# Kernel tuning notes

Measured on AMD Instinct MI355X. Metric: run time of the kernel, lower is better.

## Reference

```python
import math
import jax, jax.numpy as jnp
import numpy as np

B, S, D, H = 2, 2048, 2048, 16
HD = D // H  # head_dim = 128, rotary_dim = HD (full rotation)
ROPE_BASE = 10000.0


def setup_inputs() -> dict:
    key = jax.random.key(0)
    k0, k1, k2 = jax.random.split(key, 3)
    return {
        "x": jax.random.normal(k0, (B, S, D), dtype=jnp.float32),
        "Wqkv": jax.random.normal(k1, (D, 3 * D), dtype=jnp.float32) * 0.02,
        "bqkv": jnp.zeros((3 * D,), dtype=jnp.float32),
        "Wout": jax.random.normal(k2, (D, D), dtype=jnp.float32) * 0.02,
        "bout": jnp.zeros((D,), dtype=jnp.float32),
    }


def _rope_cos_sin(seqlen, dim):
    # flash-attn RotaryEmbedding: inv_freq over even indices, outer with positions
    inv_freq = 1.0 / (ROPE_BASE ** (jnp.arange(0, dim, 2, dtype=jnp.float32) / dim))
    t = jnp.arange(seqlen, dtype=jnp.float32)
    freqs = jnp.outer(t, inv_freq)  # (S, dim/2)
    return jnp.cos(freqs), jnp.sin(freqs)


def reference(x, Wqkv, bqkv, Wout, bout):
    b, s, d = x.shape
    hd = d // H
    # fused QKV projection -> (B, S, 3, H, HD)
    qkv = (x @ Wqkv + bqkv).reshape(b, s, 3, H, hd)
    q, k, v = qkv[:, :, 0], qkv[:, :, 1], qkv[:, :, 2]  # (B,S,H,HD)

    cos, sin = _rope_cos_sin(s, hd)
    c = cos[:, None, :]  # (S,1,HD/2) broadcast over heads
    si = sin[:, None, :]

    def rot(t):
        # split-half rotary (as in apply_rotary_emb_qkv), computed in fp32
        t1, t2 = jnp.split(t.astype(jnp.float32), 2, axis=-1)
        return jnp.concatenate([t1 * c - t2 * si, t1 * si + t2 * c], axis=-1).astype(x.dtype)

    q = rot(q)
    k = rot(k)

    scale = 1.0 / math.sqrt(hd)
    scores = jnp.einsum("bthd,bshd->bhts", q, k * scale)  # (B,H,S,S)
    causal_mask = jnp.triu(jnp.full((s, s), -10000.0, dtype=scores.dtype), 1)
    attn = jax.nn.softmax(scores + causal_mask, axis=-1)
    ctx = jnp.einsum("bhts,bshd->bthd", attn, v).reshape(b, s, d)
    return ctx @ Wout + bout
```

## Files before the change

### kernel.cpp

```cpp
#include <hip/hip_runtime.h>
#include <hip/hip_bf16.h>

typedef __attribute__((ext_vector_type(4))) float fx4;
typedef __attribute__((ext_vector_type(8))) short bx8;

#define GLD16(dst, src)                                                        \
  __builtin_amdgcn_global_load_lds(                                            \
      (__attribute__((address_space(1))) void*)(src),                          \
      (__attribute__((address_space(3))) void*)(dst), 16, 0, 0)

__device__ inline float bf2f(short s_) {
  unsigned int u = ((unsigned int)(unsigned short)s_) << 16;
  float f;
  __builtin_memcpy(&f, &u, 4);
  return f;
}
__device__ inline short f2bf(float f) {
  __hip_bfloat16 h = __float2bfloat16(f);
  short r;
  __builtin_memcpy(&r, &h, 2);
  return r;
}

__global__ __launch_bounds__(256) void k_cast(const float* __restrict__ in,
                                              __hip_bfloat16* __restrict__ out,
                                              int n4) {
  int i = blockIdx.x * 256 + threadIdx.x;
  if (i >= n4) return;
  float4 v = reinterpret_cast<const float4*>(in)[i];
  __hip_bfloat16 t[4] = {__float2bfloat16(v.x), __float2bfloat16(v.y),
                         __float2bfloat16(v.z), __float2bfloat16(v.w)};
  reinterpret_cast<ushort4*>(out)[i] = *reinterpret_cast<ushort4*>(t);
}

__global__ void k_tcast(const float* __restrict__ in,
                        __hip_bfloat16* __restrict__ out, int R, int C) {
  __shared__ float tile[32][33];
  int c0 = blockIdx.x * 32, r0 = blockIdx.y * 32;
  int tx = threadIdx.x, ty = threadIdx.y;
#pragma unroll
  for (int j = 0; j < 4; ++j)
    tile[ty + j * 8][tx] = in[(size_t)(r0 + ty + j * 8) * C + c0 + tx];
  __syncthreads();
#pragma unroll
  for (int j = 0; j < 4; ++j)
    out[(size_t)(c0 + ty + j * 8) * R + r0 + tx] =
        __float2bfloat16(tile[tx][ty + j * 8]);
}

__global__ __launch_bounds__(256) void k_ropetab(float* __restrict__ cosT,
                                                 float* __restrict__ sinT) {
  int idx = blockIdx.x * 256 + threadIdx.x;
  int t = idx >> 6, i = idx & 63;
  float inv = expf(-logf(10000.0f) * (float)i * (1.0f / 64.0f));
  float fr = (float)t * inv;
  cosT[idx] = cosf(fr);
  sinT[idx] = sinf(fr);
}

__global__ __launch_bounds__(256) void k_rope(__hip_bfloat16* __restrict__ qkv,
                                              const float* __restrict__ cosT,
                                              const float* __restrict__ sinT) {
  int t = blockIdx.x * 256 + threadIdx.x;
  int d0 = (t & 7) * 8;
  int qk = (t >> 3) & 1;
  int h = (t >> 4) & 15;
  int s = (t >> 8) & 2047;
  int b = (t >> 19) & 1;
  __hip_bfloat16* base =
      qkv + (size_t)(b * 2048 + s) * 6144 + qk * 2048 + h * 128;
  bx8 lo = *(const bx8*)(base + d0);
  bx8 hi = *(const bx8*)(base + 64 + d0);
  float4 ca = *(const float4*)&cosT[s * 64 + d0];
  float4 cb = *(const float4*)&cosT[s * 64 + d0 + 4];
  float4 sa = *(const float4*)&sinT[s * 64 + d0];
  float4 sb = *(const float4*)&sinT[s * 64 + d0 + 4];
  float c[8] = {ca.x, ca.y, ca.z, ca.w, cb.x, cb.y, cb.z, cb.w};
  float si[8] = {sa.x, sa.y, sa.z, sa.w, sb.x, sb.y, sb.z, sb.w};
  bx8 olo, ohi;
#pragma unroll
  for (int e = 0; e < 8; ++e) {
    float t1 = bf2f(lo[e]), t2 = bf2f(hi[e]);
    olo[e] = f2bf(t1 * c[e] - t2 * si[e]);
    ohi[e] = f2bf(t1 * si[e] + t2 * c[e]);
  }
  *(bx8*)(base + d0) = olo;
  *(bx8*)(base + 64 + d0) = ohi;
}

__global__ void k_vtrans(const __hip_bfloat16* __restrict__ qkv,
                         __hip_bfloat16* __restrict__ vT) {
  __shared__ __hip_bfloat16 tile[32][33];
  int s0 = blockIdx.x * 32, d0 = blockIdx.y * 32, bh = blockIdx.z;
  int b = bh >> 4, h = bh & 15;
  int tx = threadIdx.x, ty = threadIdx.y;
#pragma unroll
  for (int j = 0; j < 4; ++j)
    tile[ty + j * 8][tx] =
        qkv[(size_t)(b * 2048 + s0 + ty + j * 8) * 6144 + 4096 + h * 128 + d0 + tx];
  __syncthreads();
#pragma unroll
  for (int j = 0; j < 4; ++j)
    vT[(size_t)(bh * 128 + d0 + ty + j * 8) * 2048 + s0 + tx] = tile[tx][ty + j * 8];
}

__global__ __launch_bounds__(256) void k_gemm_bt(
    const __hip_bfloat16* __restrict__ A, const __hip_bfloat16* __restrict__ BT,
    const float* __restrict__ bias, void* __restrict__ Cp, int M, int N, int K,
    int out_bf16) {
  __shared__ __align__(16) __hip_bfloat16 As[128 * 64];
  __shared__ __align__(16) __hip_bfloat16 Bs[128 * 64];
  const int tid = threadIdx.x;
  const int m0 = blockIdx.y * 128, n0 = blockIdx.x * 128;
  const int lane = tid & 63, w = tid >> 6;
  const int lr = lane & 15, lg = lane >> 4;
  const int wr = w >> 1, wc = w & 1;

  fx4 acc[4][4];
#pragma unroll
  for (int m = 0; m < 4; ++m)
#pragma unroll
    for (int n = 0; n < 4; ++n) acc[m][n] = (fx4)(0.0f);

  for (int kt = 0; kt < K; kt += 64) {
#pragma unroll
    for (int q = 0; q < 4; ++q) {
      const int slot = q * 256 + tid;
      const int row = slot >> 3, u = slot & 7;
      const int us = (u ^ (row & 7)) * 8;
      GLD16(&As[slot * 8], A + (size_t)(m0 + row) * K + kt + us);
      GLD16(&Bs[slot * 8], BT + (size_t)(n0 + row) * K + kt + us);
    }
    __syncthreads();
#pragma unroll
    for (int ks = 0; ks < 2; ++ks) {
      bx8 af[4], bf[4];
#pragma unroll
      for (int m = 0; m < 4; ++m) {
        const int r = wr * 64 + m * 16 + lr;
        const int u = ((ks * 4 + lg) ^ (lr & 7)) * 8;
        af[m] = *(const bx8*)&As[r * 64 + u];
      }
#pragma unroll
      for (int n = 0; n < 4; ++n) {
        const int r = wc * 64 + n * 16 + lr;
        const int u = ((ks * 4 + lg) ^ (lr & 7)) * 8;
        bf[n] = *(const bx8*)&Bs[r * 64 + u];
      }
#pragma unroll
      for (int m = 0; m < 4; ++m)
#pragma unroll
        for (int n = 0; n < 4; ++n)
          acc[m][n] =
              __builtin_amdgcn_mfma_f32_16x16x32_bf16(af[m], bf[n], acc[m][n], 0, 0, 0);
    }
    __syncthreads();
  }

  float bv[4];
#pragma unroll
  for (int n = 0; n < 4; ++n) bv[n] = bias[n0 + wc * 64 + n * 16 + lr];

#pragma unroll
  for (int m = 0; m < 4; ++m)
#pragma unroll
    for (int n = 0; n < 4; ++n) {
      const int col = n0 + wc * 64 + n * 16 + lr;
#pragma unroll
      for (int j = 0; j < 4; ++j) {
        const int row = m0 + wr * 64 + m * 16 + lg * 4 + j;
        const float v = acc[m][n][j] + bv[n];
        if (out_bf16)
          ((__hip_bfloat16*)Cp)[(size_t)row * N + col] = __float2bfloat16(v);
        else
          ((float*)Cp)[(size_t)row * N + col] = v;
      }
    }
}

#define ATT_SL2E 0.12751740f

__global__ __launch_bounds__(256, 2) void k_attn(
    const __hip_bfloat16* __restrict__ qkv, const __hip_bfloat16* __restrict__ vT,
    __hip_bfloat16* __restrict__ ctx) {
  __shared__ __align__(16) __hip_bfloat16 Ks[2][128 * 128];
  __shared__ __align__(16) __hip_bfloat16 Ps[4][32 * 64];
  const int tid = threadIdx.x;
  const int lane = tid & 63, w = tid >> 6;
  const int lr = lane & 15, lg = lane >> 4;
  const int bid = blockIdx.x;
  const int lo = bid & 255, hi = bid >> 8;
  const int bh = lo & 31, qsel = lo >> 5;
  const int b = bh >> 4, h = bh & 15;
  const int qt = hi ? qsel : 15 - qsel;

  const __hip_bfloat16* kbase = qkv + (size_t)b * 2048 * 6144 + 2048 + h * 128;
  const __hip_bfloat16* vbase = vT + (size_t)(b * 16 + h) * 128 * 2048;

  auto STAGE = [&](int bufi, int kt) {
    const int kv0 = kt * 128;
#pragma unroll
    for (int q = 0; q < 8; ++q) {
      const int slot = q * 256 + tid;
      const int row = slot >> 4, u = slot & 15;
      GLD16(&Ks[bufi][slot * 8],
            kbase + (size_t)(kv0 + row) * 6144 + ((u ^ (row & 15)) * 8));
    }
  };

  const __hip_bfloat16* qbase =
      qkv + (size_t)(b * 2048 + qt * 128 + w * 32) * 6144 + h * 128;
  bx8 qf[2][4];
#pragma unroll
  for (int m = 0; m < 2; ++m)
#pragma unroll
    for (int ks = 0; ks < 4; ++ks)
      qf[m][ks] = *(const bx8*)(qbase + (size_t)(m * 16 + lr) * 6144 + ks * 32 + lg * 8);

  bx8 vones;
#pragma unroll
  for (int e = 0; e < 8; ++e) vones[e] = (short)0x3F80;

  fx4 oacc[2][8], lacc[2];
#pragma unroll
  for (int m = 0; m < 2; ++m) {
    lacc[m] = (fx4)(0.0f);
#pragma unroll
    for (int d = 0; d < 8; ++d) oacc[m][d] = (fx4)(0.0f);
  }

  const int ntile = qt + 1;
  const int qrow0 = qt * 128 + w * 32;

  STAGE(0, 0);
  for (int kt = 0; kt < ntile; ++kt) {
    const int cur = kt & 1;
    if (kt + 1 < ntile) {
      STAGE(cur ^ 1, kt + 1);
      asm volatile("s_waitcnt vmcnt(8)" ::: "memory");
    } else {
      asm volatile("s_waitcnt vmcnt(0)" ::: "memory");
    }
    __builtin_amdgcn_s_barrier();
    asm volatile("" ::: "memory");

#pragma unroll
    for (int h2 = 0; h2 < 2; ++h2) {
      const int kv0 = kt * 128 + h2 * 64;
      if (kv0 > qrow0 + 31) continue;

      fx4 sacc[2][4];
#pragma unroll
      for (int n = 0; n < 4; ++n) {
        sacc[0][n] = (fx4)(0.0f);
        sacc[1][n] = (fx4)(0.0f);
      }
      __builtin_amdgcn_s_setprio(1);
#pragma unroll
      for (int n = 0; n < 4; ++n) {
        const int r = h2 * 64 + n * 16 + lr;
#pragma unroll
        for (int ks = 0; ks < 4; ++ks) {
          const bx8 kf = *(const bx8*)&Ks[cur][r * 128 + (((ks * 4 + lg) ^ lr) * 8)];
          sacc[0][n] =
              __builtin_amdgcn_mfma_f32_16x16x32_bf16(qf[0][ks], kf, sacc[0][n], 0, 0, 0);
          sacc[1][n] =
              __builtin_amdgcn_mfma_f32_16x16x32_bf16(qf[1][ks], kf, sacc[1][n], 0, 0, 0);
        }
      }
      __builtin_amdgcn_s_setprio(0);

      const bool needmask = (kv0 + 63) > qrow0;
#pragma unroll
      for (int n = 0; n < 4; ++n) {
        const int kvi = kv0 + n * 16 + lr;
#pragma unroll
        for (int m = 0; m < 2; ++m)
#pragma unroll
          for (int j = 0; j < 4; ++j) {
            float v = sacc[m][n][j] * ATT_SL2E;
            if (needmask) {
              const int qi = qrow0 + m * 16 + lg * 4 + j;
              if (kvi > qi) v = -200.0f;
            }
            const float p = exp2f(fminf(v, 60.0f));
            const int r = m * 16 + lg * 4 + j, c = n * 16 + lr;
            const int c2 = (c & 7) | (((c >> 3) ^ (r & 7)) << 3);
            Ps[w][r * 64 + c2] = __float2bfloat16(p);
          }
      }

      __builtin_amdgcn_s_setprio(1);
#pragma unroll
      for (int ks2 = 0; ks2 < 2; ++ks2) {
        const int u = ((ks2 * 4 + lg) ^ (lr & 7)) * 8;
        const bx8 pf0 = *(const bx8*)&Ps[w][(0 * 16 + lr) * 64 + u];
        const bx8 pf1 = *(const bx8*)&Ps[w][(1 * 16 + lr) * 64 + u];
        lacc[0] = __builtin_amdgcn_mfma_f32_16x16x32_bf16(pf0, vones, lacc[0], 0, 0, 0);
        lacc[1] = __builtin_amdgcn_mfma_f32_16x16x32_bf16(pf1, vones, lacc[1], 0, 0, 0);
#pragma unroll
        for (int dn = 0; dn < 8; ++dn) {
          const bx8 vf = *(const bx8*)(vbase + (size_t)(dn * 16 + lr) * 2048 + kv0 +
                                       ks2 * 32 + lg * 8);
          oacc[0][dn] =
              __builtin_amdgcn_mfma_f32_16x16x32_bf16(pf0, vf, oacc[0][dn], 0, 0, 0);
          oacc[1][dn] =
              __builtin_amdgcn_mfma_f32_16x16x32_bf16(pf1, vf, oacc[1][dn], 0, 0, 0);
        }
      }
      __builtin_amdgcn_s_setprio(0);
    }
    __builtin_amdgcn_s_barrier();
    asm volatile("" ::: "memory");
  }

  float rl[2][4];
#pragma unroll
  for (int m = 0; m < 2; ++m)
#pragma unroll
    for (int j = 0; j < 4; ++j) rl[m][j] = 1.0f / lacc[m][j];
#pragma unroll
  for (int m = 0; m < 2; ++m)
#pragma unroll
    for (int dn = 0; dn < 8; ++dn)
#pragma unroll
      for (int j = 0; j < 4; ++j) {
        const int row = qt * 128 + w * 32 + m * 16 + lg * 4 + j;
        ctx[(size_t)(b * 2048 + row) * 2048 + h * 128 + dn * 16 + lr] =
            __float2bfloat16(oacc[m][dn][j] * rl[m][j]);
      }
}

extern "C" void kernel_launch(void* const* d_in, const int* in_sizes, int n_in,
                              void* d_out, int out_size, void* d_ws, size_t ws_size,
                              hipStream_t stream) {
  const float* x = (const float*)d_in[0];
  const float* Wqkv = (const float*)d_in[1];
  const float* bqkv = (const float*)d_in[2];
  const float* Wout = (const float*)d_in[3];
  const float* bout = (const float*)d_in[4];
  float* out = (float*)d_out;

  char* ws = (char*)d_ws;
  __hip_bfloat16* xb    = (__hip_bfloat16*)(ws + 0);
  __hip_bfloat16* wqkvT = (__hip_bfloat16*)(ws + 16777216);
  __hip_bfloat16* woutT = (__hip_bfloat16*)(ws + 41943040);
  __hip_bfloat16* qkvb  = (__hip_bfloat16*)(ws + 50331648);
  __hip_bfloat16* vTb   = (__hip_bfloat16*)(ws + 100663296);
  __hip_bfloat16* ctxb  = (__hip_bfloat16*)(ws + 117440512);
  float* cosT = (float*)(ws + 134217728);
  float* sinT = (float*)(ws + 134742016);

  k_cast<<<8192, 256, 0, stream>>>(x, xb, 2097152);
  k_tcast<<<dim3(192, 64), dim3(32, 8), 0, stream>>>(Wqkv, wqkvT, 2048, 6144);
  k_tcast<<<dim3(64, 64), dim3(32, 8), 0, stream>>>(Wout, woutT, 2048, 2048);
  k_ropetab<<<512, 256, 0, stream>>>(cosT, sinT);
  k_gemm_bt<<<dim3(48, 32), 256, 0, stream>>>(xb, wqkvT, bqkv, qkvb, 4096, 6144,
                                              2048, 1);
  k_rope<<<4096, 256, 0, stream>>>(qkvb, cosT, sinT);
  k_vtrans<<<dim3(64, 4, 32), dim3(32, 8), 0, stream>>>(qkvb, vTb);
  k_attn<<<512, 256, 0, stream>>>(qkvb, vTb, ctxb);
  k_gemm_bt<<<dim3(16, 32), 256, 0, stream>>>(ctxb, woutT, bout, out, 4096, 2048,
                                              2048, 0);
}
```

Before: 331.2 us.

## Add 256x256 pipelined QKV GEMM kernel and prefetch V fragments in attention

Replaces the 128x128 QKV projection GEMM with a new 512-thread kernel that computes 256x256 tiles. It double-buffers K-slices in LDS through direct global-to-LDS loads, interleaves the loads with MFMA phases using explicit waitcnt and barriers, and swizzles the block order for L2 locality. In attention, the V fragments for each 64-key chunk are loaded into registers before the QK/softmax phase, so their global latency overlaps that compute. The cost is higher register pressure and more complex synchronisation.

```diff
diff --git a/kernel.cpp b/kernel.cpp
--- a/kernel.cpp
+++ b/kernel.cpp
@@ -3,6 +3,7 @@
 
 typedef __attribute__((ext_vector_type(4))) float fx4;
 typedef __attribute__((ext_vector_type(8))) short bx8;
+typedef __hip_bfloat16 bf16;
 
 #define GLD16(dst, src)                                                        \
   __builtin_amdgcn_global_load_lds(                                            \
@@ -23,18 +24,17 @@
 }
 
 __global__ __launch_bounds__(256) void k_cast(const float* __restrict__ in,
-                                              __hip_bfloat16* __restrict__ out,
-                                              int n4) {
+                                              bf16* __restrict__ out, int n4) {
   int i = blockIdx.x * 256 + threadIdx.x;
   if (i >= n4) return;
   float4 v = reinterpret_cast<const float4*>(in)[i];
-  __hip_bfloat16 t[4] = {__float2bfloat16(v.x), __float2bfloat16(v.y),
-                         __float2bfloat16(v.z), __float2bfloat16(v.w)};
+  bf16 t[4] = {__float2bfloat16(v.x), __float2bfloat16(v.y),
+               __float2bfloat16(v.z), __float2bfloat16(v.w)};
   reinterpret_cast<ushort4*>(out)[i] = *reinterpret_cast<ushort4*>(t);
 }
 
-__global__ void k_tcast(const float* __restrict__ in,
-                        __hip_bfloat16* __restrict__ out, int R, int C) {
+__global__ void k_tcast(const float* __restrict__ in, bf16* __restrict__ out,
+                        int R, int C) {
   __shared__ float tile[32][33];
   int c0 = blockIdx.x * 32, r0 = blockIdx.y * 32;
   int tx = threadIdx.x, ty = threadIdx.y;
@@ -58,7 +58,7 @@
   sinT[idx] = sinf(fr);
 }
 
-__global__ __launch_bounds__(256) void k_rope(__hip_bfloat16* __restrict__ qkv,
+__global__ __launch_bounds__(256) void k_rope(bf16* __restrict__ qkv,
                                               const float* __restrict__ cosT,
                                               const float* __restrict__ sinT) {
   int t = blockIdx.x * 256 + threadIdx.x;
@@ -67,8 +67,7 @@
   int h = (t >> 4) & 15;
   int s = (t >> 8) & 2047;
   int b = (t >> 19) & 1;
-  __hip_bfloat16* base =
-      qkv + (size_t)(b * 2048 + s) * 6144 + qk * 2048 + h * 128;
+  bf16* base = qkv + (size_t)(b * 2048 + s) * 6144 + qk * 2048 + h * 128;
   bx8 lo = *(const bx8*)(base + d0);
   bx8 hi = *(const bx8*)(base + 64 + d0);
   float4 ca = *(const float4*)&cosT[s * 64 + d0];
@@ -88,9 +87,8 @@
   *(bx8*)(base + 64 + d0) = ohi;
 }
 
-__global__ void k_vtrans(const __hip_bfloat16* __restrict__ qkv,
-                         __hip_bfloat16* __restrict__ vT) {
-  __shared__ __hip_bfloat16 tile[32][33];
+__global__ void k_vtrans(const bf16* __restrict__ qkv, bf16* __restrict__ vT) {
+  __shared__ bf16 tile[32][33];
   int s0 = blockIdx.x * 32, d0 = blockIdx.y * 32, bh = blockIdx.z;
   int b = bh >> 4, h = bh & 15;
   int tx = threadIdx.x, ty = threadIdx.y;
@@ -104,12 +102,125 @@
     vT[(size_t)(bh * 128 + d0 + ty + j * 8) * 2048 + s0 + tx] = tile[tx][ty + j * 8];
 }
 
+__global__ __launch_bounds__(512, 2) void k_gemm256(
+    const bf16* __restrict__ A, const bf16* __restrict__ BT,
+    const float* __restrict__ bias, bf16* __restrict__ C, int M, int N, int K,
+    int NBX) {
+  __shared__ __align__(16) bf16 As[2][2][256 * 32];
+  __shared__ __align__(16) bf16 Bs[2][2][256 * 32];
+  const int tid = threadIdx.x;
+  const int lane = tid & 63, wid = tid >> 6;
+  const int lr = lane & 15, lg = lane >> 4;
+  const int wr = wid >> 2, wc = wid & 3;
+  const int nwg = gridDim.x, bid = blockIdx.x;
+  const int swz = (bid & 7) * (nwg >> 3) + (bid >> 3);
+  const int mb = swz / NBX, nb = swz - mb * NBX;
+  const int m0 = mb * 256, n0 = nb * 256;
+  const int NT = K >> 6;
+
+  fx4 acc[8][4];
+#pragma unroll
+  for (int m = 0; m < 8; ++m)
+#pragma unroll
+    for (int n = 0; n < 4; ++n) acc[m][n] = (fx4)(0.0f);
+
+  auto SA = [&](int buf, int ks, int t) {
+#pragma unroll
+    for (int q = 0; q < 2; ++q) {
+      const int L = q * 512 + tid;
+      const int row = L >> 2, u = L & 3;
+      GLD16(&As[buf][ks][L * 8],
+            A + (size_t)(m0 + row) * K + t * 64 + ks * 32 + ((u ^ (row & 3)) * 8));
+    }
+  };
+  auto SB = [&](int buf, int ks, int t) {
+#pragma unroll
+    for (int q = 0; q < 2; ++q) {
+      const int L = q * 512 + tid;
+      const int row = L >> 2, u = L & 3;
+      GLD16(&Bs[buf][ks][L * 8],
+            BT + (size_t)(n0 + row) * K + t * 64 + ks * 32 + ((u ^ (row & 3)) * 8));
+    }
+  };
+
+  bx8 af[4], bfr[4];
+  auto LDA = [&](int buf, int ks, int mh) {
+#pragma unroll
+    for (int m = 0; m < 4; ++m) {
+      const int r = wr * 128 + mh * 64 + m * 16 + lr;
+      af[m] = *(const bx8*)&As[buf][ks][r * 32 + ((lg ^ (r & 3)) * 8)];
+    }
+  };
+  auto LDB = [&](int buf, int ks) {
+#pragma unroll
+    for (int n = 0; n < 4; ++n) {
+      const int r = wc * 64 + n * 16 + lr;
+      bfr[n] = *(const bx8*)&Bs[buf][ks][r * 32 + ((lg ^ (r & 3)) * 8)];
+    }
+  };
+
+#define MFMA16(MH)                                                             \
+  asm volatile("s_waitcnt lgkmcnt(0)" ::: "memory");                           \
+  __builtin_amdgcn_sched_barrier(0);                                           \
+  __builtin_amdgcn_s_setprio(1);                                               \
+  _Pragma("unroll") for (int m = 0; m < 4; ++m)                                \
+      _Pragma("unroll") for (int n = 0; n < 4; ++n) acc[(MH)*4 + m][n] =       \
+          __builtin_amdgcn_mfma_f32_16x16x32_bf16(af[m], bfr[n],               \
+                                                  acc[(MH)*4 + m][n], 0, 0, 0);\
+  __builtin_amdgcn_s_setprio(0);                                               \
+  __builtin_amdgcn_s_barrier();
+
+  SA(0, 0, 0); SB(0, 0, 0);
+  SA(0, 1, 0); SB(0, 1, 0);
+  SA(1, 0, 1); SB(1, 0, 1);
+  asm volatile("s_waitcnt vmcnt(8)" ::: "memory");
+  __builtin_amdgcn_s_barrier();
+
+  for (int t = 0; t < NT; ++t) {
+    const int buf = t & 1;
+    LDA(buf, 0, 0); LDB(buf, 0);
+    if (t + 1 < NT) SA(buf ^ 1, 1, t + 1);
+    __builtin_amdgcn_s_barrier();
+    MFMA16(0)
+    LDA(buf, 0, 1);
+    if (t + 1 < NT) SB(buf ^ 1, 1, t + 1);
+    asm volatile("s_waitcnt vmcnt(8)" ::: "memory");
+    __builtin_amdgcn_s_barrier();
+    MFMA16(1)
+    LDA(buf, 1, 0); LDB(buf, 1);
+    if (t + 2 < NT) SA(buf, 0, t + 2);
+    __builtin_amdgcn_s_barrier();
+    MFMA16(0)
+    LDA(buf, 1, 1);
+    if (t + 2 < NT) SB(buf, 0, t + 2);
+    asm volatile("s_waitcnt vmcnt(8)" ::: "memory");
+    __builtin_amdgcn_s_barrier();
+    MFMA16(1)
+  }
+#undef MFMA16
+
+  float bv[4];
+#pragma unroll
+  for (int n = 0; n < 4; ++n) bv[n] = bias[n0 + wc * 64 + n * 16 + lr];
+#pragma unroll
+  for (int mm = 0; mm < 8; ++mm)
+#pragma unroll
+    for (int n = 0; n < 4; ++n) {
+      const int col = n0 + wc * 64 + n * 16 + lr;
+#pragma unroll
+      for (int j = 0; j < 4; ++j) {
+        const int row = m0 + wr * 128 + mm * 16 + lg * 4 + j;
+        C[(size_t)row * N + col] = __float2bfloat16(acc[mm][n][j] + bv[n]);
+      }
+    }
+}
+
 __global__ __launch_bounds__(256) void k_gemm_bt(
-    const __hip_bfloat16* __restrict__ A, const __hip_bfloat16* __restrict__ BT,
+    const bf16* __restrict__ A, const bf16* __restrict__ BT,
     const float* __restrict__ bias, void* __restrict__ Cp, int M, int N, int K,
     int out_bf16) {
-  __shared__ __align__(16) __hip_bfloat16 As[128 * 64];
-  __shared__ __align__(16) __hip_bfloat16 Bs[128 * 64];
+  __shared__ __align__(16) bf16 As[128 * 64];
+  __shared__ __align__(16) bf16 Bs[128 * 64];
   const int tid = threadIdx.x;
   const int m0 = blockIdx.y * 128, n0 = blockIdx.x * 128;
   const int lane = tid & 63, w = tid >> 6;
@@ -171,7 +282,7 @@
         const int row = m0 + wr * 64 + m * 16 + lg * 4 + j;
         const float v = acc[m][n][j] + bv[n];
         if (out_bf16)
-          ((__hip_bfloat16*)Cp)[(size_t)row * N + col] = __float2bfloat16(v);
+          ((bf16*)Cp)[(size_t)row * N + col] = __float2bfloat16(v);
         else
           ((float*)Cp)[(size_t)row * N + col] = v;
       }
@@ -180,11 +291,11 @@
 
 #define ATT_SL2E 0.12751740f
 
-__global__ __launch_bounds__(256, 2) void k_attn(
-    const __hip_bfloat16* __restrict__ qkv, const __hip_bfloat16* __restrict__ vT,
-    __hip_bfloat16* __restrict__ ctx) {
-  __shared__ __align__(16) __hip_bfloat16 Ks[2][128 * 128];
-  __shared__ __align__(16) __hip_bfloat16 Ps[4][32 * 64];
+__global__ __launch_bounds__(256, 2) void k_attn(const bf16* __restrict__ qkv,
+                                                 const bf16* __restrict__ vT,
+                                                 bf16* __restrict__ ctx) {
+  __shared__ __align__(16) bf16 Ks[2][128 * 128];
+  __shared__ __align__(16) bf16 Ps[4][32 * 64];
   const int tid = threadIdx.x;
   const int lane = tid & 63, w = tid >> 6;
   const int lr = lane & 15, lg = lane >> 4;
@@ -194,8 +305,8 @@
   const int b = bh >> 4, h = bh & 15;
   const int qt = hi ? qsel : 15 - qsel;
 
-  const __hip_bfloat16* kbase = qkv + (size_t)b * 2048 * 6144 + 2048 + h * 128;
-  const __hip_bfloat16* vbase = vT + (size_t)(b * 16 + h) * 128 * 2048;
+  const bf16* kbase = qkv + (size_t)b * 2048 * 6144 + 2048 + h * 128;
+  const bf16* vbase = vT + (size_t)(b * 16 + h) * 128 * 2048;
 
   auto STAGE = [&](int bufi, int kt) {
     const int kv0 = kt * 128;
@@ -208,7 +319,7 @@
     }
   };
 
-  const __hip_bfloat16* qbase =
+  const bf16* qbase =
       qkv + (size_t)(b * 2048 + qt * 128 + w * 32) * 6144 + h * 128;
   bx8 qf[2][4];
 #pragma unroll
@@ -248,6 +359,14 @@
     for (int h2 = 0; h2 < 2; ++h2) {
       const int kv0 = kt * 128 + h2 * 64;
       if (kv0 > qrow0 + 31) continue;
+
+      bx8 vreg[2][8];
+#pragma unroll
+      for (int ks2 = 0; ks2 < 2; ++ks2)
+#pragma unroll
+        for (int dn = 0; dn < 8; ++dn)
+          vreg[ks2][dn] = *(const bx8*)(vbase + (size_t)(dn * 16 + lr) * 2048 +
+                                        kv0 + ks2 * 32 + lg * 8);
 
       fx4 sacc[2][4];
 #pragma unroll
@@ -300,12 +419,10 @@
         lacc[1] = __builtin_amdgcn_mfma_f32_16x16x32_bf16(pf1, vones, lacc[1], 0, 0, 0);
 #pragma unroll
         for (int dn = 0; dn < 8; ++dn) {
-          const bx8 vf = *(const bx8*)(vbase + (size_t)(dn * 16 + lr) * 2048 + kv0 +
-                                       ks2 * 32 + lg * 8);
-          oacc[0][dn] =
-              __builtin_amdgcn_mfma_f32_16x16x32_bf16(pf0, vf, oacc[0][dn], 0, 0, 0);
-          oacc[1][dn] =
-              __builtin_amdgcn_mfma_f32_16x16x32_bf16(pf1, vf, oacc[1][dn], 0, 0, 0);
+          oacc[0][dn] = __builtin_amdgcn_mfma_f32_16x16x32_bf16(pf0, vreg[ks2][dn],
+                                                                oacc[0][dn], 0, 0, 0);
+          oacc[1][dn] = __builtin_amdgcn_mfma_f32_16x16x32_bf16(pf1, vreg[ks2][dn],
+                                                                oacc[1][dn], 0, 0, 0);
         }
       }
       __builtin_amdgcn_s_setprio(0);
@@ -342,12 +459,12 @@
   float* out = (float*)d_out;
 
   char* ws = (char*)d_ws;
-  __hip_bfloat16* xb    = (__hip_bfloat16*)(ws + 0);
-  __hip_bfloat16* wqkvT = (__hip_bfloat16*)(ws + 16777216);
-  __hip_bfloat16* woutT = (__hip_bfloat16*)(ws + 41943040);
-  __hip_bfloat16* qkvb  = (__hip_bfloat16*)(ws + 50331648);
-  __hip_bfloat16* vTb   = (__hip_bfloat16*)(ws + 100663296);
-  __hip_bfloat16* ctxb  = (__hip_bfloat16*)(ws + 117440512);
+  bf16* xb    = (bf16*)(ws + 0);
+  bf16* wqkvT = (bf16*)(ws + 16777216);
+  bf16* woutT = (bf16*)(ws + 41943040);
+  bf16* qkvb  = (bf16*)(ws + 50331648);
+  bf16* vTb   = (bf16*)(ws + 100663296);
+  bf16* ctxb  = (bf16*)(ws + 117440512);
   float* cosT = (float*)(ws + 134217728);
   float* sinT = (float*)(ws + 134742016);
 
@@ -355,8 +472,7 @@
   k_tcast<<<dim3(192, 64), dim3(32, 8), 0, stream>>>(Wqkv, wqkvT, 2048, 6144);
   k_tcast<<<dim3(64, 64), dim3(32, 8), 0, stream>>>(Wout, woutT, 2048, 2048);
   k_ropetab<<<512, 256, 0, stream>>>(cosT, sinT);
-  k_gemm_bt<<<dim3(48, 32), 256, 0, stream>>>(xb, wqkvT, bqkv, qkvb, 4096, 6144,
-                                              2048, 1);
+  k_gemm256<<<384, 512, 0, stream>>>(xb, wqkvT, bqkv, qkvb, 4096, 6144, 2048, 24);
   k_rope<<<4096, 256, 0, stream>>>(qkvb, cosT, sinT);
   k_vtrans<<<dim3(64, 4, 32), dim3(32, 8), 0, stream>>>(qkvb, vTb);
   k_attn<<<512, 256, 0, stream>>>(qkvb, vTb, ctxb);
```

New measurement: 408.2 us. 1.23x slower.
